# Optimization experiments

Measured on AMD Instinct MI355X. Metric: run time of the kernel, lower is better.

The kernel has to match this reference:

```python
import jax, jax.numpy as jnp
import numpy as np

N = 100000      # nodes
E = 1600000     # edges
F_IN = 64       # num_node_features
R = 8           # num_relations
G = 256         # graphs in batch
H, C = 4, 32    # GAT heads, per-head channels
NEG_SLOPE_ATT = 0.2    # GATConv attention leaky relu
NEG_SLOPE = 0.01       # F.leaky_relu default


def setup_inputs() -> dict:
    key = jax.random.key(0)
    ks = jax.random.split(key, 12)
    init = lambda k, shape, fan: (jax.random.normal(k, shape, jnp.float32) / np.sqrt(fan).astype(np.float32))
    x = jax.random.normal(ks[0], (N, F_IN), jnp.float32)
    edge_index = jax.random.randint(ks[1], (2, E), 0, N)
    edge_type = jax.random.randint(ks[2], (E,), 0, R)
    batch = (jnp.arange(N) * G) // N  # sorted graph ids, every segment non-empty
    return dict(
        x=x, edge_index=edge_index, edge_type=edge_type, batch=batch,
        gat_w=init(ks[3], (F_IN, H * C), F_IN),
        gat_att_src=init(ks[4], (H, C), C),
        gat_att_dst=init(ks[5], (H, C), C),
        gat_bias=jnp.zeros((H * C,), jnp.float32),
        dense1_w=init(ks[6], (H * C, 16), H * C),
        dense1_b=jnp.zeros((16,), jnp.float32),
        rw1=init(ks[7], (R, F_IN, 32), F_IN),
        root1=init(ks[8], (F_IN, 32), F_IN),
        rb1=jnp.zeros((32,), jnp.float32),
        rw2=init(ks[9], (R, 32, 16), 32),
        root2=init(ks[10], (32, 16), 32),
        rb2=jnp.zeros((16,), jnp.float32),
        dense_w=init(ks[11], (32, 1), 32),
        dense_b=jnp.zeros((1,), jnp.float32),
    )


def _gat(x, src, dst, w, att_src, att_dst, bias):
    h = (x @ w).reshape(N, H, C)                       # [N,H,C]
    a_src = jnp.sum(h * att_src, axis=-1)              # [N,H]
    a_dst = jnp.sum(h * att_dst, axis=-1)              # [N,H]
    e = jax.nn.leaky_relu(a_src[src] + a_dst[dst], NEG_SLOPE_ATT)  # [E,H]
    # segment softmax over incoming edges of each dst node
    m = jax.ops.segment_max(e, dst, num_segments=N)    # [N,H]
    p = jnp.exp(e - m[dst])
    s = jax.ops.segment_sum(p, dst, num_segments=N)    # [N,H]
    alpha = p / s[dst]
    msg = h[src] * alpha[:, :, None]                   # [E,H,C]
    out = jax.ops.segment_sum(msg, dst, num_segments=N)
    return out.reshape(N, H * C) + bias


def _rgcn(x, src, dst, edge_type, w, root, bias):
    # per-relation transform of all nodes, then edge gather (PyG RGCNConv, aggr='mean')
    xw = jnp.einsum('ni,rio->rno', x, w)               # [R,N,out]
    msg = xw[edge_type, src]                           # [E,out]
    comb = dst * R + edge_type                         # mean is per (dst, relation)
    cnt = jax.ops.segment_sum(jnp.ones((E,), x.dtype), comb, num_segments=N * R)
    agg = jax.ops.segment_sum(msg / cnt[comb][:, None], dst, num_segments=N)
    return agg + x @ root + bias


def reference(x, edge_index, edge_type, batch, gat_w, gat_att_src, gat_att_dst,
              gat_bias, dense1_w, dense1_b, rw1, root1, rb1, rw2, root2, rb2,
              dense_w, dense_b):
    src, dst = edge_index[0], edge_index[1]
    # GAT branch (dropout treated as identity / eval mode)
    h = _gat(x, src, dst, gat_w, gat_att_src, gat_att_dst, gat_bias)
    h = jax.nn.leaky_relu(h, NEG_SLOPE)
    h = jax.nn.leaky_relu(h @ dense1_w + dense1_b, NEG_SLOPE)
    gmax = jax.ops.segment_max(h, batch, num_segments=G)          # [G,16]
    # RGCN branch
    z = jax.nn.relu(_rgcn(x, src, dst, edge_type, rw1, root1, rb1))
    z = jax.nn.relu(_rgcn(z, src, dst, edge_type, rw2, root2, rb2))
    nodes_per_graph = jax.ops.segment_sum(jnp.ones((N,), x.dtype), batch, num_segments=G)
    gmean = jax.ops.segment_sum(z, batch, num_segments=G) / nodes_per_graph[:, None]
    # fuse
    zc = jnp.concatenate([gmax, gmean], axis=1)                   # [G,32]
    return zc @ dense_w + dense_b                                  # [G,1]
```

## Files before the change

kernel.cpp:

```cpp
#include <hip/hip_runtime.h>
#include <hip/hip_bf16.h>

typedef __hip_bfloat16 bf16;
typedef unsigned short u16;

#define N_NODES 100000
#define N_EDGES 1600000
#define F_IN 64
#define N_REL 8
#define N_GRAPH 256
#define N_HEAD 4
#define HC 128
#define NBLK_SCAN 391

__device__ __forceinline__ float lrelu(float x, float s) { return x >= 0.f ? x : s * x; }
__device__ __forceinline__ unsigned fenc(float f) {
  unsigned b = __float_as_uint(f);
  return (b & 0x80000000u) ? ~b : (b | 0x80000000u);
}
__device__ __forceinline__ float fdec(unsigned u) {
  float v = __uint_as_float((u & 0x80000000u) ? (u & 0x7fffffffu) : ~u);
  return fmaxf(fminf(v, 3e38f), -3e38f);
}
__device__ __forceinline__ float bf2f(bf16 v) { return __bfloat162float(v); }
__device__ __forceinline__ bf16 f2bf(float v) { return __float2bfloat16(v); }
__device__ __forceinline__ float lo_bf(unsigned u) { return __uint_as_float(u << 16); }
__device__ __forceinline__ float hi_bf(unsigned u) { return __uint_as_float(u & 0xFFFF0000u); }
__device__ __forceinline__ unsigned f2bfu(float v) {
  unsigned u = __float_as_uint(v);
  return (u + 0x7FFFu + ((u >> 16) & 1u)) >> 16;
}

template<bool BF> __device__ __forceinline__ float ldf(const void* p, size_t i) {
  if (BF) { u16 v = ((const u16*)p)[i]; return __uint_as_float(((unsigned)v) << 16); }
  else    { return ((const float*)p)[i]; }
}

__global__ void k_probe(const u16* __restrict__ xr, int* __restrict__ flag) {
  int t = threadIdx.x;
  int c = 0;
  for (int i = t; i < 1024; i += 256) {
    unsigned e = (xr[i] >> 7) & 0xFFu;
    if (e >= 100u && e <= 140u) c++;
  }
  __shared__ int sc[256];
  sc[t] = c;
  __syncthreads();
  for (int s = 128; s; s >>= 1) { if (t < s) sc[t] += sc[t + s]; __syncthreads(); }
  if (t == 0) *flag = (sc[0] >= 800) ? 1 : 0;
}

template<bool BF>
__device__ __forceinline__ void gat_h_body(const void* x, const void* w, const void* att_s,
                                           const void* att_d, u16* __restrict__ h,
                                           float* __restrict__ a_src, float* __restrict__ a_dst) {
  int n = blockIdx.x, j = threadIdx.x;
  __shared__ float xs[F_IN];
  if (j < F_IN) xs[j] = ldf<BF>(x, (size_t)n * F_IN + j);
  __syncthreads();
  float acc = 0.f;
#pragma unroll
  for (int k = 0; k < F_IN; ++k) acc += xs[k] * ldf<BF>(w, (size_t)k * HC + j);
  h[(size_t)n * HC + j] = (u16)f2bfu(acc);
  float ps = acc * ldf<BF>(att_s, j);
  float pd = acc * ldf<BF>(att_d, j);
#pragma unroll
  for (int off = 16; off > 0; off >>= 1) {
    ps += __shfl_down(ps, off, 32);
    pd += __shfl_down(pd, off, 32);
  }
  if ((j & 31) == 0) {
    a_src[n * N_HEAD + (j >> 5)] = ps;
    a_dst[n * N_HEAD + (j >> 5)] = pd;
  }
}
__global__ void k_gat_h(const void* x, const void* w, const void* att_s, const void* att_d,
                        u16* h, float* a_src, float* a_dst, const int* flag) {
  if (__builtin_amdgcn_readfirstlane(*flag)) gat_h_body<true>(x, w, att_s, att_d, h, a_src, a_dst);
  else gat_h_body<false>(x, w, att_s, att_d, h, a_src, a_dst);
}

__global__ void k_hist(const int* __restrict__ ei, const int* __restrict__ etype,
                       int* __restrict__ deg, int* __restrict__ cnt) {
  int e = blockIdx.x * 256 + threadIdx.x;
  if (e >= N_EDGES) return;
  int d = ei[N_EDGES + e], t = etype[e];
  atomicAdd(&deg[d], 1);
  atomicAdd(&cnt[d * N_REL + t], 1);
}

__global__ void k_scan_a(const int* __restrict__ deg, int* __restrict__ rowptr,
                         int* __restrict__ scanblk) {
  __shared__ int buf[256];
  int tid = threadIdx.x;
  int i = blockIdx.x * 256 + tid;
  int v = (i < N_NODES) ? deg[i] : 0;
  buf[tid] = v;
  __syncthreads();
  for (int st = 1; st < 256; st <<= 1) {
    int t = buf[tid];
    int a = (tid >= st) ? buf[tid - st] : 0;
    __syncthreads();
    buf[tid] = t + a;
    __syncthreads();
  }
  if (i < N_NODES) rowptr[i] = buf[tid] - v;
  if (tid == 255) scanblk[blockIdx.x] = buf[255];
}
__global__ void k_scan_b(int* __restrict__ scanblk) {
  __shared__ int buf[512];
  int tid = threadIdx.x;
  int v = (tid < NBLK_SCAN) ? scanblk[tid] : 0;
  buf[tid] = v;
  __syncthreads();
  for (int st = 1; st < 512; st <<= 1) {
    int t = buf[tid];
    int a = (tid >= st) ? buf[tid - st] : 0;
    __syncthreads();
    buf[tid] = t + a;
    __syncthreads();
  }
  if (tid < NBLK_SCAN) scanblk[tid] = buf[tid] - v;
}
__global__ void k_scan_c(int* __restrict__ rowptr, int* __restrict__ wp,
                         const int* __restrict__ scanblk) {
  int i = blockIdx.x * 256 + threadIdx.x;
  if (i < N_NODES) {
    int val = rowptr[i] + scanblk[blockIdx.x];
    rowptr[i] = val;
    wp[i] = val;
  } else if (i == N_NODES) {
    rowptr[N_NODES] = N_EDGES;
  }
}

__global__ void k_scatter(const int* __restrict__ ei, const int* __restrict__ etype,
                          const float* __restrict__ a_src, const float* __restrict__ a_dst,
                          int* __restrict__ wp, unsigned* __restrict__ csr,
                          float4* __restrict__ p_logit, int* __restrict__ dstarr) {
  int e = blockIdx.x * 256 + threadIdx.x;
  if (e >= N_EDGES) return;
  int sn = ei[e], d = ei[N_EDGES + e], t = etype[e];
  int pos = atomicAdd(&wp[d], 1);
  csr[pos] = (unsigned)sn | ((unsigned)t << 20);
  dstarr[pos] = d;
  const float4 as = *(const float4*)&a_src[sn * 4];
  const float4 ad = *(const float4*)&a_dst[d * 4];
  float4 lg;
  lg.x = lrelu(as.x + ad.x, 0.2f);
  lg.y = lrelu(as.y + ad.y, 0.2f);
  lg.z = lrelu(as.z + ad.z, 0.2f);
  lg.w = lrelu(as.w + ad.w, 0.2f);
  p_logit[pos] = lg;
}

__global__ void k_msum(const int* __restrict__ rowptr, const float* __restrict__ p_logit,
                       float* __restrict__ m_arr, float* __restrict__ si_arr) {
  int tid = threadIdx.x;
  int n = blockIdx.x * 16 + (tid >> 4);
  int l16 = tid & 15, head = l16 & 3, slot = l16 >> 2;
  int base = rowptr[n], deg = rowptr[n + 1] - base;
  float m = -1e30f;
  for (int i = slot; i < deg; i += 4) m = fmaxf(m, p_logit[(size_t)(base + i) * 4 + head]);
  m = fmaxf(m, __shfl_xor(m, 4, 64));
  m = fmaxf(m, __shfl_xor(m, 8, 64));
  float s = 0.f;
  for (int i = slot; i < deg; i += 4) s += __expf(p_logit[(size_t)(base + i) * 4 + head] - m);
  s += __shfl_xor(s, 4, 64);
  s += __shfl_xor(s, 8, 64);
  if (slot == 0) {
    m_arr[n * 4 + head] = m;
    si_arr[n * 4 + head] = (deg > 0) ? 1.f / s : 0.f;
  }
}

__global__ void k_alpha(const int* __restrict__ dstarr, const float* __restrict__ m_arr,
                        const float* __restrict__ si_arr, float4* __restrict__ plog4) {
  int p = blockIdx.x * 256 + threadIdx.x;
  if (p >= N_EDGES) return;
  int d = dstarr[p];
  float4 lg = plog4[p];
  const float4 m4 = *(const float4*)&m_arr[d * 4];
  const float4 s4 = *(const float4*)&si_arr[d * 4];
  float4 a;
  a.x = __expf(lg.x - m4.x) * s4.x;
  a.y = __expf(lg.y - m4.y) * s4.y;
  a.z = __expf(lg.z - m4.z) * s4.z;
  a.w = __expf(lg.w - m4.w) * s4.w;
  plog4[p] = a;
}

template<bool BF>
__device__ __forceinline__ void gat_agg_body(const int* __restrict__ rowptr,
                                             const unsigned* __restrict__ csr,
                                             const float* __restrict__ alpha,
                                             const uint2* __restrict__ hu2, const void* gbias,
                                             const void* d1w, const void* d1b,
                                             const int* __restrict__ batch,
                                             unsigned* __restrict__ gmax, int* __restrict__ npg) {
  int tid = threadIdx.x;
  int wave = tid >> 6, l = tid & 63;
  int d = blockIdx.x * 4 + wave;
  __shared__ float os[4][132];
  int base = rowptr[d];
  int deg = rowptr[d + 1] - base;
  int slot = l >> 5, cl = l & 31;
  int head = cl >> 3;
  float a0 = 0.f, a1 = 0.f, a2 = 0.f, a3 = 0.f;
  int i = slot;
  for (; i + 6 < deg; i += 8) {
    unsigned sp0 = csr[base + i],     sp1 = csr[base + i + 2];
    unsigned sp2 = csr[base + i + 4], sp3 = csr[base + i + 6];
    float av0 = alpha[(size_t)(base + i) * 4 + head];
    float av1 = alpha[(size_t)(base + i + 2) * 4 + head];
    float av2 = alpha[(size_t)(base + i + 4) * 4 + head];
    float av3 = alpha[(size_t)(base + i + 6) * 4 + head];
    uint2 h0 = hu2[(size_t)(sp0 & 0xFFFFF) * 32 + cl];
    uint2 h1 = hu2[(size_t)(sp1 & 0xFFFFF) * 32 + cl];
    uint2 h2 = hu2[(size_t)(sp2 & 0xFFFFF) * 32 + cl];
    uint2 h3 = hu2[(size_t)(sp3 & 0xFFFFF) * 32 + cl];
    a0 += lo_bf(h0.x) * av0 + lo_bf(h1.x) * av1 + lo_bf(h2.x) * av2 + lo_bf(h3.x) * av3;
    a1 += hi_bf(h0.x) * av0 + hi_bf(h1.x) * av1 + hi_bf(h2.x) * av2 + hi_bf(h3.x) * av3;
    a2 += lo_bf(h0.y) * av0 + lo_bf(h1.y) * av1 + lo_bf(h2.y) * av2 + lo_bf(h3.y) * av3;
    a3 += hi_bf(h0.y) * av0 + hi_bf(h1.y) * av1 + hi_bf(h2.y) * av2 + hi_bf(h3.y) * av3;
  }
  for (; i < deg; i += 2) {
    unsigned sp = csr[base + i];
    float av = alpha[(size_t)(base + i) * 4 + head];
    uint2 hv = hu2[(size_t)(sp & 0xFFFFF) * 32 + cl];
    a0 += lo_bf(hv.x) * av;
    a1 += hi_bf(hv.x) * av;
    a2 += lo_bf(hv.y) * av;
    a3 += hi_bf(hv.y) * av;
  }
  a0 += __shfl_xor(a0, 32, 64);
  a1 += __shfl_xor(a1, 32, 64);
  a2 += __shfl_xor(a2, 32, 64);
  a3 += __shfl_xor(a3, 32, 64);
  if (slot == 0) {
    os[wave][4 * cl + 0] = lrelu(a0 + ldf<BF>(gbias, 4 * cl + 0), 0.01f);
    os[wave][4 * cl + 1] = lrelu(a1 + ldf<BF>(gbias, 4 * cl + 1), 0.01f);
    os[wave][4 * cl + 2] = lrelu(a2 + ldf<BF>(gbias, 4 * cl + 2), 0.01f);
    os[wave][4 * cl + 3] = lrelu(a3 + ldf<BF>(gbias, 4 * cl + 3), 0.01f);
  }
  __syncthreads();
  if (tid < 64) {
    int node = tid >> 4, out = tid & 15;
    float acc = ldf<BF>(d1b, out);
#pragma unroll
    for (int k = 0; k < HC; ++k) acc += os[node][k] * ldf<BF>(d1w, (size_t)k * 16 + out);
    acc = lrelu(acc, 0.01f);
    atomicMax(&gmax[batch[blockIdx.x * 4 + node] * 16 + out], fenc(acc));
  }
  if (tid < 4) atomicAdd(&npg[batch[blockIdx.x * 4 + tid]], 1);
}
__global__ void k_gat_agg(const int* rowptr, const unsigned* csr, const float* alpha,
                          const u16* h, const void* gbias, const void* d1w, const void* d1b,
                          const int* batch, unsigned* gmax, int* npg, const int* flag) {
  if (__builtin_amdgcn_readfirstlane(*flag))
    gat_agg_body<true>(rowptr, csr, alpha, (const uint2*)h, gbias, d1w, d1b, batch, gmax, npg);
  else
    gat_agg_body<false>(rowptr, csr, alpha, (const uint2*)h, gbias, d1w, d1b, batch, gmax, npg);
}

template<bool BF>
__device__ __forceinline__ void xw1_body(const void* x, const void* rw1, bf16* __restrict__ xw1) {
  __shared__ float xs[8][F_IN];
  int tid = threadIdx.x;
  int n0 = blockIdx.x * 8;
  for (int i = tid; i < 8 * F_IN; i += 256) {
    int nn = n0 + (i >> 6);
    xs[i >> 6][i & 63] = (nn < N_NODES) ? ldf<BF>(x, (size_t)nn * F_IN + (i & 63)) : 0.f;
  }
  __syncthreads();
  int nl = tid >> 5, c = tid & 31;
  int n = n0 + nl, r = blockIdx.y;
  float acc = 0.f;
#pragma unroll
  for (int k = 0; k < F_IN; ++k) acc += xs[nl][k] * ldf<BF>(rw1, (size_t)(r * F_IN + k) * 32 + c);
  if (n < N_NODES) xw1[((size_t)r * N_NODES + n) * 32 + c] = f2bf(acc);
}
__global__ void k_xw1(const void* x, const void* rw1, bf16* xw1, const int* flag) {
  if (__builtin_amdgcn_readfirstlane(*flag)) xw1_body<true>(x, rw1, xw1);
  else xw1_body<false>(x, rw1, xw1);
}

template<bool BF>
__device__ __forceinline__ void ragg1_body(const int* __restrict__ rowptr,
                                           const unsigned* __restrict__ csr,
                                           const int* __restrict__ cnt,
                                           const u16* __restrict__ xw, const void* x,
                                           const void* root1, const void* rb1,
                                           float* __restrict__ z1) {
  __shared__ float xs[4][F_IN];
  __shared__ float cinv[4][N_REL];
  int tid = threadIdx.x;
  int n0 = blockIdx.x * 4;
  {
    int nn = n0 + (tid >> 6);
    xs[tid >> 6][tid & 63] = ldf<BF>(x, (size_t)nn * F_IN + (tid & 63));
  }
  if (tid < 32) {
    int cv = cnt[(n0 + (tid >> 3)) * N_REL + (tid & 7)];
    cinv[tid >> 3][tid & 7] = (cv > 0) ? 1.f / (float)cv : 0.f;
  }
  __syncthreads();
  int wave = tid >> 6, l = tid & 63;
  int half = l >> 5, c = l & 31;
  int n = n0 + wave;
  int base = rowptr[n], deg = rowptr[n + 1] - base;
  float acc = 0.f;
  int i = half;
  for (; i + 2 < deg; i += 4) {
    unsigned sp0 = csr[base + i], sp1 = csr[base + i + 2];
    int t0 = sp0 >> 20, t1 = sp1 >> 20;
    u16 v0 = xw[((size_t)t0 * N_NODES + (sp0 & 0xFFFFF)) * 32 + c];
    u16 v1 = xw[((size_t)t1 * N_NODES + (sp1 & 0xFFFFF)) * 32 + c];
    acc += __uint_as_float(((unsigned)v0) << 16) * cinv[wave][t0];
    acc += __uint_as_float(((unsigned)v1) << 16) * cinv[wave][t1];
  }
  if (i < deg) {
    unsigned sp = csr[base + i];
    int t = sp >> 20;
    u16 v = xw[((size_t)t * N_NODES + (sp & 0xFFFFF)) * 32 + c];
    acc += __uint_as_float(((unsigned)v) << 16) * cinv[wave][t];
  }
  float r = 0.f;
#pragma unroll
  for (int kk = 0; kk < 32; ++kk) {
    int k = half * 32 + kk;
    r += xs[wave][k] * ldf<BF>(root1, (size_t)k * 32 + c);
  }
  float tot = acc + r;
  tot += __shfl_xor(tot, 32, 64);
  if (half == 0) z1[(size_t)n * 32 + c] = fmaxf(tot + ldf<BF>(rb1, c), 0.f);
}
__global__ void k_ragg1(const int* rowptr, const unsigned* csr, const int* cnt,
                        const bf16* xw1, const void* x, const void* root1, const void* rb1,
                        float* z1, const int* flag) {
  if (__builtin_amdgcn_readfirstlane(*flag))
    ragg1_body<true>(rowptr, csr, cnt, (const u16*)xw1, x, root1, rb1, z1);
  else
    ragg1_body<false>(rowptr, csr, cnt, (const u16*)xw1, x, root1, rb1, z1);
}

template<bool BF>
__device__ __forceinline__ void zw2_body(const float* __restrict__ z1, const void* rw2,
                                         bf16* __restrict__ zw2) {
  __shared__ float zs[16][32];
  int tid = threadIdx.x;
  int n0 = blockIdx.x * 16;
  for (int i = tid; i < 16 * 32; i += 256) {
    int nn = n0 + (i >> 5);
    zs[i >> 5][i & 31] = (nn < N_NODES) ? z1[(size_t)nn * 32 + (i & 31)] : 0.f;
  }
  __syncthreads();
  int nl = tid >> 4, c = tid & 15;
  int n = n0 + nl, r = blockIdx.y;
  float acc = 0.f;
#pragma unroll
  for (int k = 0; k < 32; ++k) acc += zs[nl][k] * ldf<BF>(rw2, (size_t)(r * 32 + k) * 16 + c);
  if (n < N_NODES) zw2[((size_t)r * N_NODES + n) * 16 + c] = f2bf(acc);
}
__global__ void k_zw2(const float* z1, const void* rw2, bf16* zw2, const int* flag) {
  if (__builtin_amdgcn_readfirstlane(*flag)) zw2_body<true>(z1, rw2, zw2);
  else zw2_body<false>(z1, rw2, zw2);
}

template<bool BF>
__device__ __forceinline__ void ragg2_body(const int* __restrict__ rowptr,
                                           const unsigned* __restrict__ csr,
                                           const int* __restrict__ cnt,
                                           const u16* __restrict__ zw,
                                           const float* __restrict__ z1, const void* root2,
                                           const void* rb2, const int* __restrict__ batch,
                                           float* __restrict__ gsum) {
  __shared__ float zs[4][33];
  __shared__ float cinv[4][N_REL];
  int tid = threadIdx.x;
  int n0 = blockIdx.x * 4;
  if (tid < 128) {
    int nn = n0 + (tid >> 5);
    zs[tid >> 5][tid & 31] = z1[(size_t)nn * 32 + (tid & 31)];
  }
  if (tid < 32) {
    int cv = cnt[(n0 + (tid >> 3)) * N_REL + (tid & 7)];
    cinv[tid >> 3][tid & 7] = (cv > 0) ? 1.f / (float)cv : 0.f;
  }
  __syncthreads();
  int wave = tid >> 6, l = tid & 63;
  int q = l >> 4, c = l & 15;
  int n = n0 + wave;
  int base = rowptr[n], deg = rowptr[n + 1] - base;
  float acc = 0.f;
  int i = q;
  for (; i + 4 < deg; i += 8) {
    unsigned sp0 = csr[base + i], sp1 = csr[base + i + 4];
    int t0 = sp0 >> 20, t1 = sp1 >> 20;
    u16 v0 = zw[((size_t)t0 * N_NODES + (sp0 & 0xFFFFF)) * 16 + c];
    u16 v1 = zw[((size_t)t1 * N_NODES + (sp1 & 0xFFFFF)) * 16 + c];
    acc += __uint_as_float(((unsigned)v0) << 16) * cinv[wave][t0];
    acc += __uint_as_float(((unsigned)v1) << 16) * cinv[wave][t1];
  }
  if (i < deg) {
    unsigned sp = csr[base + i];
    int t = sp >> 20;
    u16 v = zw[((size_t)t * N_NODES + (sp & 0xFFFFF)) * 16 + c];
    acc += __uint_as_float(((unsigned)v) << 16) * cinv[wave][t];
  }
  float r = 0.f;
#pragma unroll
  for (int kk = 0; kk < 8; ++kk) {
    int k = q * 8 + kk;
    r += zs[wave][k] * ldf<BF>(root2, (size_t)k * 16 + c);
  }
  float tot = acc + r;
  tot += __shfl_xor(tot, 16, 64);
  tot += __shfl_xor(tot, 32, 64);
  if (q == 0) {
    float z2 = fmaxf(tot + ldf<BF>(rb2, c), 0.f);
    atomicAdd(&gsum[batch[n] * 16 + c], z2);
  }
}
__global__ void k_ragg2(const int* rowptr, const unsigned* csr, const int* cnt,
                        const bf16* zw2, const float* z1, const void* root2, const void* rb2,
                        const int* batch, float* gsum, const int* flag) {
  if (__builtin_amdgcn_readfirstlane(*flag))
    ragg2_body<true>(rowptr, csr, cnt, (const u16*)zw2, z1, root2, rb2, batch, gsum);
  else
    ragg2_body<false>(rowptr, csr, cnt, (const u16*)zw2, z1, root2, rb2, batch, gsum);
}

template<bool BF>
__device__ __forceinline__ void final_body(const unsigned* __restrict__ gmax,
                                           const float* __restrict__ gsum,
                                           const int* __restrict__ npg, const void* dw,
                                           const void* db, void* out) {
  int g = threadIdx.x;
  if (g >= N_GRAPH) return;
  float acc = ldf<BF>(db, 0);
  int np = npg[g]; if (np < 1) np = 1;
  float inv = 1.f / (float)np;
#pragma unroll
  for (int c = 0; c < 16; ++c) {
    acc += fdec(gmax[g * 16 + c]) * ldf<BF>(dw, c);
    acc += (gsum[g * 16 + c] * inv) * ldf<BF>(dw, 16 + c);
  }
  if (BF) ((bf16*)out)[g] = f2bf(acc);
  else ((float*)out)[g] = acc;
}
__global__ void k_final(const unsigned* gmax, const float* gsum, const int* npg,
                        const void* dw, const void* db, void* out, const int* flag) {
  if (__builtin_amdgcn_readfirstlane(*flag)) final_body<true>(gmax, gsum, npg, dw, db, out);
  else final_body<false>(gmax, gsum, npg, dw, db, out);
}

extern "C" void kernel_launch(void* const* d_in, const int* in_sizes, int n_in,
                              void* d_out, int out_size, void* d_ws, size_t ws_size,
                              hipStream_t stream) {
  const void* x        = d_in[0];
  const int*  ei       = (const int*)d_in[1];
  const int*  etype    = (const int*)d_in[2];
  const int*  batch    = (const int*)d_in[3];
  const void* gat_w    = d_in[4];
  const void* att_src  = d_in[5];
  const void* att_dst  = d_in[6];
  const void* gat_bias = d_in[7];
  const void* d1w      = d_in[8];
  const void* d1b      = d_in[9];
  const void* rw1      = d_in[10];
  const void* root1    = d_in[11];
  const void* rb1      = d_in[12];
  const void* rw2      = d_in[13];
  const void* root2    = d_in[14];
  const void* rb2      = d_in[15];
  const void* dw       = d_in[16];
  const void* db       = d_in[17];

  char* ws = (char*)d_ws;
  const size_t o_h     = 0;
  const size_t o_plog  = 25600000;
  const size_t o_xw1   = 0;
  const size_t o_zw2   = 0;
  const size_t o_asrc  = 51200000;
  const size_t o_adst  = 52800000;
  const size_t o_deg   = 54400000;
  const size_t o_rowp  = 54800000;
  const size_t o_wp    = 55200016;
  const size_t o_cnt   = 55600032;
  const size_t o_csr   = 58800032;
  const size_t o_z1    = 65200032;
  const size_t o_sblk  = 78000032;
  const size_t o_gmax  = 78001600;
  const size_t o_gsum  = 78017984;
  const size_t o_npg   = 78034368;
  const size_t o_flag  = 78035392;
  const size_t o_dst   = 78035400;
  const size_t total   = 84435400;
  if (ws_size < total) return;

  u16*      h      = (u16*)(ws + o_h);
  float*    plog   = (float*)(ws + o_plog);
  bf16*     xw1    = (bf16*)(ws + o_xw1);
  bf16*     zw2    = (bf16*)(ws + o_zw2);
  float*    a_src  = (float*)(ws + o_asrc);
  float*    a_dst  = (float*)(ws + o_adst);
  int*      deg    = (int*)(ws + o_deg);
  int*      rowptr = (int*)(ws + o_rowp);
  int*      wp     = (int*)(ws + o_wp);
  int*      cnt    = (int*)(ws + o_cnt);
  unsigned* csr    = (unsigned*)(ws + o_csr);
  float*    z1     = (float*)(ws + o_z1);
  int*      sblk   = (int*)(ws + o_sblk);
  unsigned* gmax   = (unsigned*)(ws + o_gmax);
  float*    gsum   = (float*)(ws + o_gsum);
  int*      npg    = (int*)(ws + o_npg);
  int*      flag   = (int*)(ws + o_flag);
  int*      dstarr = (int*)(ws + o_dst);

  k_probe<<<1, 256, 0, stream>>>((const u16*)x, flag);

  hipMemsetAsync(ws + o_deg, 0, o_csr - o_deg, stream);
  hipMemsetAsync(ws + o_gmax, 0, 33792, stream);

  k_gat_h<<<N_NODES, 128, 0, stream>>>(x, gat_w, att_src, att_dst, h, a_src, a_dst, flag);

  k_hist<<<(N_EDGES + 255) / 256, 256, 0, stream>>>(ei, etype, deg, cnt);
  k_scan_a<<<NBLK_SCAN, 256, 0, stream>>>(deg, rowptr, sblk);
  k_scan_b<<<1, 512, 0, stream>>>(sblk);
  k_scan_c<<<NBLK_SCAN, 256, 0, stream>>>(rowptr, wp, sblk);
  k_scatter<<<(N_EDGES + 255) / 256, 256, 0, stream>>>(ei, etype, a_src, a_dst, wp, csr,
                                                       (float4*)plog, dstarr);

  k_msum<<<N_NODES / 16, 256, 0, stream>>>(rowptr, plog, a_src, a_dst);
  k_alpha<<<(N_EDGES + 255) / 256, 256, 0, stream>>>(dstarr, a_src, a_dst, (float4*)plog);

  k_gat_agg<<<N_NODES / 4, 256, 0, stream>>>(rowptr, csr, plog, h, gat_bias, d1w, d1b, batch,
                                             gmax, npg, flag);

  k_xw1<<<dim3((N_NODES + 7) / 8, N_REL), 256, 0, stream>>>(x, rw1, xw1, flag);
  k_ragg1<<<N_NODES / 4, 256, 0, stream>>>(rowptr, csr, cnt, xw1, x, root1, rb1, z1, flag);

  k_zw2<<<dim3((N_NODES + 15) / 16, N_REL), 256, 0, stream>>>(z1, rw2, zw2, flag);
  k_ragg2<<<N_NODES / 4, 256, 0, stream>>>(rowptr, csr, cnt, zw2, z1, root2, rb2,
                                           batch, gsum, flag);

  k_final<<<1, 256, 0, stream>>>(gmax, gsum, npg, dw, db, d_out, flag);
}
```

Measured before the change: 1.231 ms.

## Aggregate raw 64-dim features per head, then apply GAT weight after aggregation

Result: slower. 1.494 ms (+21.4%).

```diff
diff --git a/kernel.cpp b/kernel.cpp
--- a/kernel.cpp
+++ b/kernel.cpp
@@ -35,6 +35,10 @@
   if (BF) { u16 v = ((const u16*)p)[i]; return __uint_as_float(((unsigned)v) << 16); }
   else    { return ((const float*)p)[i]; }
 }
+template<bool BF> __device__ __forceinline__ float2 ldf2(const void* p, size_t i) {
+  if (BF) { unsigned v = ((const unsigned*)p)[i]; return make_float2(lo_bf(v), hi_bf(v)); }
+  else    { return ((const float2*)p)[i]; }
+}
 
 __global__ void k_probe(const u16* __restrict__ xr, int* __restrict__ flag) {
   int t = threadIdx.x;
@@ -52,16 +56,16 @@
 
 template<bool BF>
 __device__ __forceinline__ void gat_h_body(const void* x, const void* w, const void* att_s,
-                                           const void* att_d, u16* __restrict__ h,
+                                           const void* att_d, u16* __restrict__ xb,
                                            float* __restrict__ a_src, float* __restrict__ a_dst) {
   int n = blockIdx.x, j = threadIdx.x;
   __shared__ float xs[F_IN];
   if (j < F_IN) xs[j] = ldf<BF>(x, (size_t)n * F_IN + j);
   __syncthreads();
+  if (!BF && j < F_IN) xb[(size_t)n * F_IN + j] = (u16)f2bfu(xs[j]);
   float acc = 0.f;
 #pragma unroll
   for (int k = 0; k < F_IN; ++k) acc += xs[k] * ldf<BF>(w, (size_t)k * HC + j);
-  h[(size_t)n * HC + j] = (u16)f2bfu(acc);
   float ps = acc * ldf<BF>(att_s, j);
   float pd = acc * ldf<BF>(att_d, j);
 #pragma unroll
@@ -75,9 +79,9 @@
   }
 }
 __global__ void k_gat_h(const void* x, const void* w, const void* att_s, const void* att_d,
-                        u16* h, float* a_src, float* a_dst, const int* flag) {
-  if (__builtin_amdgcn_readfirstlane(*flag)) gat_h_body<true>(x, w, att_s, att_d, h, a_src, a_dst);
-  else gat_h_body<false>(x, w, att_s, att_d, h, a_src, a_dst);
+                        u16* xb, float* a_src, float* a_dst, const int* flag) {
+  if (__builtin_amdgcn_readfirstlane(*flag)) gat_h_body<true>(x, w, att_s, att_d, xb, a_src, a_dst);
+  else gat_h_body<false>(x, w, att_s, att_d, xb, a_src, a_dst);
 }
 
 __global__ void k_hist(const int* __restrict__ ei, const int* __restrict__ etype,
@@ -194,73 +198,99 @@
 __device__ __forceinline__ void gat_agg_body(const int* __restrict__ rowptr,
                                              const unsigned* __restrict__ csr,
                                              const float* __restrict__ alpha,
-                                             const uint2* __restrict__ hu2, const void* gbias,
-                                             const void* d1w, const void* d1b,
+                                             const unsigned* __restrict__ xu, const void* gat_w,
+                                             const void* gbias, const void* d1w, const void* d1b,
                                              const int* __restrict__ batch,
                                              unsigned* __restrict__ gmax, int* __restrict__ npg) {
   int tid = threadIdx.x;
   int wave = tid >> 6, l = tid & 63;
   int d = blockIdx.x * 4 + wave;
+  __shared__ float u_lds[4][4][F_IN];
   __shared__ float os[4][132];
+  const float4* alpha4 = (const float4*)alpha;
   int base = rowptr[d];
   int deg = rowptr[d + 1] - base;
   int slot = l >> 5, cl = l & 31;
-  int head = cl >> 3;
-  float a0 = 0.f, a1 = 0.f, a2 = 0.f, a3 = 0.f;
+  float acc[4][2] = {{0.f,0.f},{0.f,0.f},{0.f,0.f},{0.f,0.f}};
   int i = slot;
   for (; i + 6 < deg; i += 8) {
     unsigned sp0 = csr[base + i],     sp1 = csr[base + i + 2];
     unsigned sp2 = csr[base + i + 4], sp3 = csr[base + i + 6];
-    float av0 = alpha[(size_t)(base + i) * 4 + head];
-    float av1 = alpha[(size_t)(base + i + 2) * 4 + head];
-    float av2 = alpha[(size_t)(base + i + 4) * 4 + head];
-    float av3 = alpha[(size_t)(base + i + 6) * 4 + head];
-    uint2 h0 = hu2[(size_t)(sp0 & 0xFFFFF) * 32 + cl];
-    uint2 h1 = hu2[(size_t)(sp1 & 0xFFFFF) * 32 + cl];
-    uint2 h2 = hu2[(size_t)(sp2 & 0xFFFFF) * 32 + cl];
-    uint2 h3 = hu2[(size_t)(sp3 & 0xFFFFF) * 32 + cl];
-    a0 += lo_bf(h0.x) * av0 + lo_bf(h1.x) * av1 + lo_bf(h2.x) * av2 + lo_bf(h3.x) * av3;
-    a1 += hi_bf(h0.x) * av0 + hi_bf(h1.x) * av1 + hi_bf(h2.x) * av2 + hi_bf(h3.x) * av3;
-    a2 += lo_bf(h0.y) * av0 + lo_bf(h1.y) * av1 + lo_bf(h2.y) * av2 + lo_bf(h3.y) * av3;
-    a3 += hi_bf(h0.y) * av0 + hi_bf(h1.y) * av1 + hi_bf(h2.y) * av2 + hi_bf(h3.y) * av3;
+    float4 a0 = alpha4[base + i],     a1 = alpha4[base + i + 2];
+    float4 a2 = alpha4[base + i + 4], a3 = alpha4[base + i + 6];
+    unsigned x0 = xu[(size_t)(sp0 & 0xFFFFF) * 32 + cl];
+    unsigned x1 = xu[(size_t)(sp1 & 0xFFFFF) * 32 + cl];
+    unsigned x2 = xu[(size_t)(sp2 & 0xFFFFF) * 32 + cl];
+    unsigned x3 = xu[(size_t)(sp3 & 0xFFFFF) * 32 + cl];
+    float x0l = lo_bf(x0), x0h = hi_bf(x0), x1l = lo_bf(x1), x1h = hi_bf(x1);
+    float x2l = lo_bf(x2), x2h = hi_bf(x2), x3l = lo_bf(x3), x3h = hi_bf(x3);
+    acc[0][0] += a0.x*x0l + a1.x*x1l + a2.x*x2l + a3.x*x3l;
+    acc[0][1] += a0.x*x0h + a1.x*x1h + a2.x*x2h + a3.x*x3h;
+    acc[1][0] += a0.y*x0l + a1.y*x1l + a2.y*x2l + a3.y*x3l;
+    acc[1][1] += a0.y*x0h + a1.y*x1h + a2.y*x2h + a3.y*x3h;
+    acc[2][0] += a0.z*x0l + a1.z*x1l + a2.z*x2l + a3.z*x3l;
+    acc[2][1] += a0.z*x0h + a1.z*x1h + a2.z*x2h + a3.z*x3h;
+    acc[3][0] += a0.w*x0l + a1.w*x1l + a2.w*x2l + a3.w*x3l;
+    acc[3][1] += a0.w*x0h + a1.w*x1h + a2.w*x2h + a3.w*x3h;
   }
   for (; i < deg; i += 2) {
     unsigned sp = csr[base + i];
-    float av = alpha[(size_t)(base + i) * 4 + head];
-    uint2 hv = hu2[(size_t)(sp & 0xFFFFF) * 32 + cl];
-    a0 += lo_bf(hv.x) * av;
-    a1 += hi_bf(hv.x) * av;
-    a2 += lo_bf(hv.y) * av;
-    a3 += hi_bf(hv.y) * av;
-  }
-  a0 += __shfl_xor(a0, 32, 64);
-  a1 += __shfl_xor(a1, 32, 64);
-  a2 += __shfl_xor(a2, 32, 64);
-  a3 += __shfl_xor(a3, 32, 64);
+    float4 a0 = alpha4[base + i];
+    unsigned xv = xu[(size_t)(sp & 0xFFFFF) * 32 + cl];
+    float xl = lo_bf(xv), xh = hi_bf(xv);
+    acc[0][0] += a0.x*xl; acc[0][1] += a0.x*xh;
+    acc[1][0] += a0.y*xl; acc[1][1] += a0.y*xh;
+    acc[2][0] += a0.z*xl; acc[2][1] += a0.z*xh;
+    acc[3][0] += a0.w*xl; acc[3][1] += a0.w*xh;
+  }
+#pragma unroll
+  for (int hh = 0; hh < 4; ++hh) {
+    acc[hh][0] += __shfl_xor(acc[hh][0], 32, 64);
+    acc[hh][1] += __shfl_xor(acc[hh][1], 32, 64);
+  }
   if (slot == 0) {
-    os[wave][4 * cl + 0] = lrelu(a0 + ldf<BF>(gbias, 4 * cl + 0), 0.01f);
-    os[wave][4 * cl + 1] = lrelu(a1 + ldf<BF>(gbias, 4 * cl + 1), 0.01f);
-    os[wave][4 * cl + 2] = lrelu(a2 + ldf<BF>(gbias, 4 * cl + 2), 0.01f);
-    os[wave][4 * cl + 3] = lrelu(a3 + ldf<BF>(gbias, 4 * cl + 3), 0.01f);
+#pragma unroll
+    for (int hh = 0; hh < 4; ++hh) {
+      u_lds[wave][hh][2 * cl]     = acc[hh][0];
+      u_lds[wave][hh][2 * cl + 1] = acc[hh][1];
+    }
+  }
+  __syncthreads();
+  {
+    int node = tid >> 6, p = tid & 63;
+    int hh = p >> 4;
+    float o0 = 0.f, o1 = 0.f;
+#pragma unroll
+    for (int k = 0; k < F_IN; ++k) {
+      float2 wv = ldf2<BF>(gat_w, (size_t)k * 64 + p);
+      float uv = u_lds[node][hh][k];
+      o0 += uv * wv.x;
+      o1 += uv * wv.y;
+    }
+    os[node][2 * p]     = lrelu(o0 + ldf<BF>(gbias, 2 * p), 0.01f);
+    os[node][2 * p + 1] = lrelu(o1 + ldf<BF>(gbias, 2 * p + 1), 0.01f);
   }
   __syncthreads();
   if (tid < 64) {
     int node = tid >> 4, out = tid & 15;
-    float acc = ldf<BF>(d1b, out);
-#pragma unroll
-    for (int k = 0; k < HC; ++k) acc += os[node][k] * ldf<BF>(d1w, (size_t)k * 16 + out);
-    acc = lrelu(acc, 0.01f);
-    atomicMax(&gmax[batch[blockIdx.x * 4 + node] * 16 + out], fenc(acc));
+    float a2 = ldf<BF>(d1b, out);
+#pragma unroll
+    for (int k = 0; k < HC; ++k) a2 += os[node][k] * ldf<BF>(d1w, (size_t)k * 16 + out);
+    a2 = lrelu(a2, 0.01f);
+    atomicMax(&gmax[batch[blockIdx.x * 4 + node] * 16 + out], fenc(a2));
   }
   if (tid < 4) atomicAdd(&npg[batch[blockIdx.x * 4 + tid]], 1);
 }
 __global__ void k_gat_agg(const int* rowptr, const unsigned* csr, const float* alpha,
-                          const u16* h, const void* gbias, const void* d1w, const void* d1b,
-                          const int* batch, unsigned* gmax, int* npg, const int* flag) {
+                          const void* x_in, const u16* xb, const void* gat_w, const void* gbias,
+                          const void* d1w, const void* d1b, const int* batch,
+                          unsigned* gmax, int* npg, const int* flag) {
   if (__builtin_amdgcn_readfirstlane(*flag))
-    gat_agg_body<true>(rowptr, csr, alpha, (const uint2*)h, gbias, d1w, d1b, batch, gmax, npg);
+    gat_agg_body<true>(rowptr, csr, alpha, (const unsigned*)x_in, gat_w, gbias, d1w, d1b,
+                       batch, gmax, npg);
   else
-    gat_agg_body<false>(rowptr, csr, alpha, (const uint2*)h, gbias, d1w, d1b, batch, gmax, npg);
+    gat_agg_body<false>(rowptr, csr, alpha, (const unsigned*)xb, gat_w, gbias, d1w, d1b,
+                        batch, gmax, npg);
 }
 
 template<bool BF>
@@ -478,7 +508,6 @@
   const void* db       = d_in[17];
 
   char* ws = (char*)d_ws;
-  const size_t o_h     = 0;
   const size_t o_plog  = 25600000;
   const size_t o_xw1   = 0;
   const size_t o_zw2   = 0;
@@ -496,10 +525,10 @@
   const size_t o_npg   = 78034368;
   const size_t o_flag  = 78035392;
   const size_t o_dst   = 78035400;
-  const size_t total   = 84435400;
+  const size_t o_xb    = 84435400;
+  const size_t total   = 97235400;
   if (ws_size < total) return;
 
-  u16*      h      = (u16*)(ws + o_h);
   float*    plog   = (float*)(ws + o_plog);
   bf16*     xw1    = (bf16*)(ws + o_xw1);
   bf16*     zw2    = (bf16*)(ws + o_zw2);
@@ -517,13 +546,14 @@
   int*      npg    = (int*)(ws + o_npg);
   int*      flag   = (int*)(ws + o_flag);
   int*      dstarr = (int*)(ws + o_dst);
+  u16*      xb     = (u16*)(ws + o_xb);
 
   k_probe<<<1, 256, 0, stream>>>((const u16*)x, flag);
 
   hipMemsetAsync(ws + o_deg, 0, o_csr - o_deg, stream);
   hipMemsetAsync(ws + o_gmax, 0, 33792, stream);
 
-  k_gat_h<<<N_NODES, 128, 0, stream>>>(x, gat_w, att_src, att_dst, h, a_src, a_dst, flag);
+  k_gat_h<<<N_NODES, 128, 0, stream>>>(x, gat_w, att_src, att_dst, xb, a_src, a_dst, flag);
 
   k_hist<<<(N_EDGES + 255) / 256, 256, 0, stream>>>(ei, etype, deg, cnt);
   k_scan_a<<<NBLK_SCAN, 256, 0, stream>>>(deg, rowptr, sblk);
@@ -535,8 +565,8 @@
   k_msum<<<N_NODES / 16, 256, 0, stream>>>(rowptr, plog, a_src, a_dst);
   k_alpha<<<(N_EDGES + 255) / 256, 256, 0, stream>>>(dstarr, a_src, a_dst, (float4*)plog);
 
-  k_gat_agg<<<N_NODES / 4, 256, 0, stream>>>(rowptr, csr, plog, h, gat_bias, d1w, d1b, batch,
-                                             gmax, npg, flag);
+  k_gat_agg<<<N_NODES / 4, 256, 0, stream>>>(rowptr, csr, plog, x, xb, gat_w, gat_bias,
+                                             d1w, d1b, batch, gmax, npg, flag);
 
   k_xw1<<<dim3((N_NODES + 7) / 8, N_REL), 256, 0, stream>>>(x, rw1, xw1, flag);
   k_ragg1<<<N_NODES / 4, 256, 0, stream>>>(rowptr, csr, cnt, xw1, x, root1, rb1, z1, flag);
```

## Co-schedule independent kernels in merged launches and vectorize RGCN gathers

Applied to the files above, without the earlier changes.

Result: no change. 1.230 ms (-0.1%).

```diff
diff --git a/kernel.cpp b/kernel.cpp
--- a/kernel.cpp
+++ b/kernel.cpp
@@ -35,6 +35,10 @@
   if (BF) { u16 v = ((const u16*)p)[i]; return __uint_as_float(((unsigned)v) << 16); }
   else    { return ((const float*)p)[i]; }
 }
+template<bool BF> __device__ __forceinline__ float2 ldf2(const void* p, size_t i) {
+  if (BF) { unsigned v = ((const unsigned*)p)[i]; return make_float2(lo_bf(v), hi_bf(v)); }
+  else    { return ((const float2*)p)[i]; }
+}
 
 __global__ void k_probe(const u16* __restrict__ xr, int* __restrict__ flag) {
   int t = threadIdx.x;
@@ -53,9 +57,9 @@
 template<bool BF>
 __device__ __forceinline__ void gat_h_body(const void* x, const void* w, const void* att_s,
                                            const void* att_d, u16* __restrict__ h,
-                                           float* __restrict__ a_src, float* __restrict__ a_dst) {
-  int n = blockIdx.x, j = threadIdx.x;
-  __shared__ float xs[F_IN];
+                                           float* __restrict__ a_src, float* __restrict__ a_dst,
+                                           int n, float* xs) {
+  int j = threadIdx.x;
   if (j < F_IN) xs[j] = ldf<BF>(x, (size_t)n * F_IN + j);
   __syncthreads();
   float acc = 0.f;
@@ -74,19 +78,25 @@
     a_dst[n * N_HEAD + (j >> 5)] = pd;
   }
 }
-__global__ void k_gat_h(const void* x, const void* w, const void* att_s, const void* att_d,
-                        u16* h, float* a_src, float* a_dst, const int* flag) {
-  if (__builtin_amdgcn_readfirstlane(*flag)) gat_h_body<true>(x, w, att_s, att_d, h, a_src, a_dst);
-  else gat_h_body<false>(x, w, att_s, att_d, h, a_src, a_dst);
-}
-
-__global__ void k_hist(const int* __restrict__ ei, const int* __restrict__ etype,
-                       int* __restrict__ deg, int* __restrict__ cnt) {
-  int e = blockIdx.x * 256 + threadIdx.x;
-  if (e >= N_EDGES) return;
-  int d = ei[N_EDGES + e], t = etype[e];
-  atomicAdd(&deg[d], 1);
-  atomicAdd(&cnt[d * N_REL + t], 1);
+
+__global__ void k_gath_hist(const void* x, const void* w, const void* att_s, const void* att_d,
+                            u16* h, float* a_src, float* a_dst,
+                            const int* __restrict__ ei, const int* __restrict__ etype,
+                            int* __restrict__ deg, int* __restrict__ cnt, const int* flag) {
+  __shared__ float xs[F_IN];
+  if (blockIdx.x < N_NODES) {
+    if (__builtin_amdgcn_readfirstlane(*flag))
+      gat_h_body<true>(x, w, att_s, att_d, h, a_src, a_dst, blockIdx.x, xs);
+    else
+      gat_h_body<false>(x, w, att_s, att_d, h, a_src, a_dst, blockIdx.x, xs);
+  } else {
+    int e = (blockIdx.x - N_NODES) * 128 + threadIdx.x;
+    if (e < N_EDGES) {
+      int d = ei[N_EDGES + e], t = etype[e];
+      atomicAdd(&deg[d], 1);
+      atomicAdd(&cnt[d * N_REL + t], 1);
+    }
+  }
 }
 
 __global__ void k_scan_a(const int* __restrict__ deg, int* __restrict__ rowptr,
@@ -197,11 +207,11 @@
                                              const uint2* __restrict__ hu2, const void* gbias,
                                              const void* d1w, const void* d1b,
                                              const int* __restrict__ batch,
-                                             unsigned* __restrict__ gmax, int* __restrict__ npg) {
+                                             unsigned* __restrict__ gmax, int* __restrict__ npg,
+                                             float (*os)[132], int bid) {
   int tid = threadIdx.x;
   int wave = tid >> 6, l = tid & 63;
-  int d = blockIdx.x * 4 + wave;
-  __shared__ float os[4][132];
+  int d = bid * 4 + wave;
   int base = rowptr[d];
   int deg = rowptr[d + 1] - base;
   int slot = l >> 5, cl = l & 31;
@@ -250,46 +260,53 @@
 #pragma unroll
     for (int k = 0; k < HC; ++k) acc += os[node][k] * ldf<BF>(d1w, (size_t)k * 16 + out);
     acc = lrelu(acc, 0.01f);
-    atomicMax(&gmax[batch[blockIdx.x * 4 + node] * 16 + out], fenc(acc));
-  }
-  if (tid < 4) atomicAdd(&npg[batch[blockIdx.x * 4 + tid]], 1);
-}
-__global__ void k_gat_agg(const int* rowptr, const unsigned* csr, const float* alpha,
-                          const u16* h, const void* gbias, const void* d1w, const void* d1b,
-                          const int* batch, unsigned* gmax, int* npg, const int* flag) {
-  if (__builtin_amdgcn_readfirstlane(*flag))
-    gat_agg_body<true>(rowptr, csr, alpha, (const uint2*)h, gbias, d1w, d1b, batch, gmax, npg);
-  else
-    gat_agg_body<false>(rowptr, csr, alpha, (const uint2*)h, gbias, d1w, d1b, batch, gmax, npg);
-}
-
-template<bool BF>
-__device__ __forceinline__ void xw1_body(const void* x, const void* rw1, bf16* __restrict__ xw1) {
-  __shared__ float xs[8][F_IN];
-  int tid = threadIdx.x;
-  int n0 = blockIdx.x * 8;
+    atomicMax(&gmax[batch[bid * 4 + node] * 16 + out], fenc(acc));
+  }
+  if (tid < 4) atomicAdd(&npg[batch[bid * 4 + tid]], 1);
+}
+
+template<bool BF>
+__device__ __forceinline__ void xw1_body(const void* x, const void* rw1, bf16* __restrict__ xw1,
+                                         int n0, int r, float (*xs)[F_IN]) {
+  int tid = threadIdx.x;
   for (int i = tid; i < 8 * F_IN; i += 256) {
     int nn = n0 + (i >> 6);
     xs[i >> 6][i & 63] = (nn < N_NODES) ? ldf<BF>(x, (size_t)nn * F_IN + (i & 63)) : 0.f;
   }
   __syncthreads();
   int nl = tid >> 5, c = tid & 31;
-  int n = n0 + nl, r = blockIdx.y;
+  int n = n0 + nl;
   float acc = 0.f;
 #pragma unroll
   for (int k = 0; k < F_IN; ++k) acc += xs[nl][k] * ldf<BF>(rw1, (size_t)(r * F_IN + k) * 32 + c);
   if (n < N_NODES) xw1[((size_t)r * N_NODES + n) * 32 + c] = f2bf(acc);
 }
-__global__ void k_xw1(const void* x, const void* rw1, bf16* xw1, const int* flag) {
-  if (__builtin_amdgcn_readfirstlane(*flag)) xw1_body<true>(x, rw1, xw1);
-  else xw1_body<false>(x, rw1, xw1);
+
+__global__ void k_aggxw1(const int* rowptr, const unsigned* csr, const float* alpha,
+                         const u16* h, const void* gbias, const void* d1w, const void* d1b,
+                         const int* batch, unsigned* gmax, int* npg,
+                         const void* x, const void* rw1, bf16* xw1, const int* flag) {
+  __shared__ float sh[544];
+  int bf = __builtin_amdgcn_readfirstlane(*flag);
+  if (blockIdx.x < 25000) {
+    if (bf) gat_agg_body<true>(rowptr, csr, alpha, (const uint2*)h, gbias, d1w, d1b,
+                               batch, gmax, npg, (float(*)[132])sh, blockIdx.x);
+    else    gat_agg_body<false>(rowptr, csr, alpha, (const uint2*)h, gbias, d1w, d1b,
+                                batch, gmax, npg, (float(*)[132])sh, blockIdx.x);
+  } else {
+    int nb = blockIdx.x - 25000;
+    int n0 = (nb % 12500) * 8;
+    int r  = nb / 12500;
+    if (bf) xw1_body<true>(x, rw1, xw1, n0, r, (float(*)[F_IN])sh);
+    else    xw1_body<false>(x, rw1, xw1, n0, r, (float(*)[F_IN])sh);
+  }
 }
 
 template<bool BF>
 __device__ __forceinline__ void ragg1_body(const int* __restrict__ rowptr,
                                            const unsigned* __restrict__ csr,
                                            const int* __restrict__ cnt,
-                                           const u16* __restrict__ xw, const void* x,
+                                           const unsigned* __restrict__ xw, const void* x,
                                            const void* root1, const void* rb1,
                                            float* __restrict__ z1) {
   __shared__ float xs[4][F_IN];
@@ -306,42 +323,50 @@
   }
   __syncthreads();
   int wave = tid >> 6, l = tid & 63;
-  int half = l >> 5, c = l & 31;
+  int slot = l >> 4, cl = l & 15;
   int n = n0 + wave;
   int base = rowptr[n], deg = rowptr[n + 1] - base;
-  float acc = 0.f;
-  int i = half;
-  for (; i + 2 < deg; i += 4) {
-    unsigned sp0 = csr[base + i], sp1 = csr[base + i + 2];
+  float a0 = 0.f, a1 = 0.f;
+  int i = slot;
+  for (; i + 4 < deg; i += 8) {
+    unsigned sp0 = csr[base + i], sp1 = csr[base + i + 4];
     int t0 = sp0 >> 20, t1 = sp1 >> 20;
-    u16 v0 = xw[((size_t)t0 * N_NODES + (sp0 & 0xFFFFF)) * 32 + c];
-    u16 v1 = xw[((size_t)t1 * N_NODES + (sp1 & 0xFFFFF)) * 32 + c];
-    acc += __uint_as_float(((unsigned)v0) << 16) * cinv[wave][t0];
-    acc += __uint_as_float(((unsigned)v1) << 16) * cinv[wave][t1];
+    unsigned v0 = xw[((size_t)t0 * N_NODES + (sp0 & 0xFFFFF)) * 16 + cl];
+    unsigned v1 = xw[((size_t)t1 * N_NODES + (sp1 & 0xFFFFF)) * 16 + cl];
+    float c0 = cinv[wave][t0], c1 = cinv[wave][t1];
+    a0 += lo_bf(v0) * c0 + lo_bf(v1) * c1;
+    a1 += hi_bf(v0) * c0 + hi_bf(v1) * c1;
   }
   if (i < deg) {
     unsigned sp = csr[base + i];
     int t = sp >> 20;
-    u16 v = xw[((size_t)t * N_NODES + (sp & 0xFFFFF)) * 32 + c];
-    acc += __uint_as_float(((unsigned)v) << 16) * cinv[wave][t];
-  }
-  float r = 0.f;
-#pragma unroll
-  for (int kk = 0; kk < 32; ++kk) {
-    int k = half * 32 + kk;
-    r += xs[wave][k] * ldf<BF>(root1, (size_t)k * 32 + c);
-  }
-  float tot = acc + r;
-  tot += __shfl_xor(tot, 32, 64);
-  if (half == 0) z1[(size_t)n * 32 + c] = fmaxf(tot + ldf<BF>(rb1, c), 0.f);
+    unsigned v = xw[((size_t)t * N_NODES + (sp & 0xFFFFF)) * 16 + cl];
+    float c0 = cinv[wave][t];
+    a0 += lo_bf(v) * c0;
+    a1 += hi_bf(v) * c0;
+  }
+#pragma unroll
+  for (int kk = 0; kk < 16; ++kk) {
+    int k = slot * 16 + kk;
+    float xv = xs[wave][k];
+    float2 wv = ldf2<BF>(root1, (size_t)k * 16 + cl);
+    a0 += xv * wv.x;
+    a1 += xv * wv.y;
+  }
+  a0 += __shfl_xor(a0, 16, 64); a0 += __shfl_xor(a0, 32, 64);
+  a1 += __shfl_xor(a1, 16, 64); a1 += __shfl_xor(a1, 32, 64);
+  if (slot == 0) {
+    z1[(size_t)n * 32 + 2 * cl]     = fmaxf(a0 + ldf<BF>(rb1, 2 * cl), 0.f);
+    z1[(size_t)n * 32 + 2 * cl + 1] = fmaxf(a1 + ldf<BF>(rb1, 2 * cl + 1), 0.f);
+  }
 }
 __global__ void k_ragg1(const int* rowptr, const unsigned* csr, const int* cnt,
                         const bf16* xw1, const void* x, const void* root1, const void* rb1,
                         float* z1, const int* flag) {
   if (__builtin_amdgcn_readfirstlane(*flag))
-    ragg1_body<true>(rowptr, csr, cnt, (const u16*)xw1, x, root1, rb1, z1);
+    ragg1_body<true>(rowptr, csr, cnt, (const unsigned*)xw1, x, root1, rb1, z1);
   else
-    ragg1_body<false>(rowptr, csr, cnt, (const u16*)xw1, x, root1, rb1, z1);
+    ragg1_body<false>(rowptr, csr, cnt, (const unsigned*)xw1, x, root1, rb1, z1);
 }
 
 template<bool BF>
@@ -371,7 +396,7 @@
 __device__ __forceinline__ void ragg2_body(const int* __restrict__ rowptr,
                                            const unsigned* __restrict__ csr,
                                            const int* __restrict__ cnt,
-                                           const u16* __restrict__ zw,
+                                           const unsigned* __restrict__ zw,
                                            const float* __restrict__ z1, const void* root2,
                                            const void* rb2, const int* __restrict__ batch,
                                            float* __restrict__ gsum) {
@@ -389,46 +414,53 @@
   }
   __syncthreads();
   int wave = tid >> 6, l = tid & 63;
-  int q = l >> 4, c = l & 15;
+  int slot = l >> 3, cl = l & 7;
   int n = n0 + wave;
   int base = rowptr[n], deg = rowptr[n + 1] - base;
-  float acc = 0.f;
-  int i = q;
-  for (; i + 4 < deg; i += 8) {
-    unsigned sp0 = csr[base + i], sp1 = csr[base + i + 4];
+  float a0 = 0.f, a1 = 0.f;
+  int i = slot;
+  for (; i + 8 < deg; i += 16) {
+    unsigned sp0 = csr[base + i], sp1 = csr[base + i + 8];
     int t0 = sp0 >> 20, t1 = sp1 >> 20;
-    u16 v0 = zw[((size_t)t0 * N_NODES + (sp0 & 0xFFFFF)) * 16 + c];
-    u16 v1 = zw[((size_t)t1 * N_NODES + (sp1 & 0xFFFFF)) * 16 + c];
-    acc += __uint_as_float(((unsigned)v0) << 16) * cinv[wave][t0];
-    acc += __uint_as_float(((unsigned)v1) << 16) * cinv[wave][t1];
+    unsigned v0 = zw[((size_t)t0 * N_NODES + (sp0 & 0xFFFFF)) * 8 + cl];
+    unsigned v1 = zw[((size_t)t1 * N_NODES + (sp1 & 0xFFFFF)) * 8 + cl];
+    float c0 = cinv[wave][t0], c1 = cinv[wave][t1];
+    a0 += lo_bf(v0) * c0 + lo_bf(v1) * c1;
+    a1 += hi_bf(v0) * c0 + hi_bf(v1) * c1;
   }
   if (i < deg) {
     unsigned sp = csr[base + i];
     int t = sp >> 20;
-    u16 v = zw[((size_t)t * N_NODES + (sp & 0xFFFFF)) * 16 + c];
-    acc += __uint_as_float(((unsigned)v) << 16) * cinv[wave][t];
-  }
-  float r = 0.f;
-#pragma unroll
-  for (int kk = 0; kk < 8; ++kk) {
-    int k = q * 8 + kk;
-    r += zs[wave][k] * ldf<BF>(root2, (size_t)k * 16 + c);
-  }
-  float tot = acc + r;
-  tot += __shfl_xor(tot, 16, 64);
-  tot += __shfl_xor(tot, 32, 64);
-  if (q == 0) {
-    float z2 = fmaxf(tot + ldf<BF>(rb2, c), 0.f);
-    atomicAdd(&gsum[batch[n] * 16 + c], z2);
+    unsigned v = zw[((size_t)t * N_NODES + (sp & 0xFFFFF)) * 8 + cl];
+    float c0 = cinv[wave][t];
+    a0 += lo_bf(v) * c0;
+    a1 += hi_bf(v) * c0;
+  }
+#pragma unroll
+  for (int kk = 0; kk < 4; ++kk) {
+    int k = slot * 4 + kk;
+    float zv = zs[wave][k];
+    float2 wv = ldf2<BF>(root2, (size_t)k * 8 + cl);
+    a0 += zv * wv.x;
+    a1 += zv * wv.y;
+  }
+  a0 += __shfl_xor(a0, 8, 64); a0 += __shfl_xor(a0, 16, 64); a0 += __shfl_xor(a0, 32, 64);
+  a1 += __shfl_xor(a1, 8, 64); a1 += __shfl_xor(a1, 16, 64); a1 += __shfl_xor(a1, 32, 64);
+  if (slot == 0) {
+    float z2a = fmaxf(a0 + ldf<BF>(rb2, 2 * cl), 0.f);
+    float z2b = fmaxf(a1 + ldf<BF>(rb2, 2 * cl + 1), 0.f);
+    int g = batch[n];
+    atomicAdd(&gsum[g * 16 + 2 * cl], z2a);
+    atomicAdd(&gsum[g * 16 + 2 * cl + 1], z2b);
   }
 }
 __global__ void k_ragg2(const int* rowptr, const unsigned* csr, const int* cnt,
                         const bf16* zw2, const float* z1, const void* root2, const void* rb2,
                         const int* batch, float* gsum, const int* flag) {
   if (__builtin_amdgcn_readfirstlane(*flag))
-    ragg2_body<true>(rowptr, csr, cnt, (const u16*)zw2, z1, root2, rb2, batch, gsum);
+    ragg2_body<true>(rowptr, csr, cnt, (const unsigned*)zw2, z1, root2, rb2, batch, gsum);
   else
-    ragg2_body<false>(rowptr, csr, cnt, (const u16*)zw2, z1, root2, rb2, batch, gsum);
+    ragg2_body<false>(rowptr, csr, cnt, (const unsigned*)zw2, z1, root2, rb2, batch, gsum);
 }
 
 template<bool BF>
@@ -480,28 +512,29 @@
   char* ws = (char*)d_ws;
   const size_t o_h     = 0;
   const size_t o_plog  = 25600000;
-  const size_t o_xw1   = 0;
+  const size_t o_xw1   = 51200000;
+  const size_t o_dst   = 51200000;
   const size_t o_zw2   = 0;
-  const size_t o_asrc  = 51200000;
-  const size_t o_adst  = 52800000;
-  const size_t o_deg   = 54400000;
-  const size_t o_rowp  = 54800000;
-  const size_t o_wp    = 55200016;
-  const size_t o_cnt   = 55600032;
-  const size_t o_csr   = 58800032;
-  const size_t o_z1    = 65200032;
-  const size_t o_sblk  = 78000032;
-  const size_t o_gmax  = 78001600;
-  const size_t o_gsum  = 78017984;
-  const size_t o_npg   = 78034368;
-  const size_t o_flag  = 78035392;
-  const size_t o_dst   = 78035400;
-  const size_t total   = 84435400;
+  const size_t o_asrc  = 102400000;
+  const size_t o_adst  = 104000000;
+  const size_t o_deg   = 105600000;
+  const size_t o_rowp  = 106000000;
+  const size_t o_wp    = 106400016;
+  const size_t o_cnt   = 106800016;
+  const size_t o_csr   = 110000016;
+  const size_t o_z1    = 116400016;
+  const size_t o_sblk  = 129200016;
+  const size_t o_gmax  = 129201600;
+  const size_t o_gsum  = 129217984;
+  const size_t o_npg   = 129234368;
+  const size_t o_flag  = 129235392;
+  const size_t total   = 129235396;
   if (ws_size < total) return;
 
   u16*      h      = (u16*)(ws + o_h);
   float*    plog   = (float*)(ws + o_plog);
   bf16*     xw1    = (bf16*)(ws + o_xw1);
+  int*      dstarr = (int*)(ws + o_dst);
   bf16*     zw2    = (bf16*)(ws + o_zw2);
   float*    a_src  = (float*)(ws + o_asrc);
   float*    a_dst  = (float*)(ws + o_adst);
@@ -516,16 +549,15 @@
   float*    gsum   = (float*)(ws + o_gsum);
   int*      npg    = (int*)(ws + o_npg);
   int*      flag   = (int*)(ws + o_flag);
-  int*      dstarr = (int*)(ws + o_dst);
 
   k_probe<<<1, 256, 0, stream>>>((const u16*)x, flag);
 
   hipMemsetAsync(ws + o_deg, 0, o_csr - o_deg, stream);
   hipMemsetAsync(ws + o_gmax, 0, 33792, stream);
 
-  k_gat_h<<<N_NODES, 128, 0, stream>>>(x, gat_w, att_src, att_dst, h, a_src, a_dst, flag);
-
-  k_hist<<<(N_EDGES + 255) / 256, 256, 0, stream>>>(ei, etype, deg, cnt);
+  k_gath_hist<<<N_NODES + 12500, 128, 0, stream>>>(x, gat_w, att_src, att_dst, h, a_src, a_dst,
+                                                   ei, etype, deg, cnt, flag);
+
   k_scan_a<<<NBLK_SCAN, 256, 0, stream>>>(deg, rowptr, sblk);
   k_scan_b<<<1, 512, 0, stream>>>(sblk);
   k_scan_c<<<NBLK_SCAN, 256, 0, stream>>>(rowptr, wp, sblk);
@@ -535,10 +567,9 @@
   k_msum<<<N_NODES / 16, 256, 0, stream>>>(rowptr, plog, a_src, a_dst);
   k_alpha<<<(N_EDGES + 255) / 256, 256, 0, stream>>>(dstarr, a_src, a_dst, (float4*)plog);
 
-  k_gat_agg<<<N_NODES / 4, 256, 0, stream>>>(rowptr, csr, plog, h, gat_bias, d1w, d1b, batch,
-                                             gmax, npg, flag);
-
-  k_xw1<<<dim3((N_NODES + 7) / 8, N_REL), 256, 0, stream>>>(x, rw1, xw1, flag);
+  k_aggxw1<<<25000 + 100000, 256, 0, stream>>>(rowptr, csr, plog, h, gat_bias, d1w, d1b,
+                                               batch, gmax, npg, x, rw1, xw1, flag);
+
   k_ragg1<<<N_NODES / 4, 256, 0, stream>>>(rowptr, csr, cnt, xw1, x, root1, rb1, z1, flag);
 
   k_zw2<<<dim3((N_NODES + 15) / 16, N_REL), 256, 0, stream>>>(z1, rw2, zw2, flag);
```
